# Kernel optimization log

Measured on AMD Instinct MI355X. Metric: run time of the kernel, lower is better.

## Reference

```python
import jax, jax.numpy as jnp
import numpy as np

B, T, F, H, P, HEADS = 1024, 128, 9, 256, 2048, 4
DH = H // HEADS

def _lstm_layer(x, Wih, Whh, bih, bhh):
    # x: [B,T,in]; gate order i,f,g,o (torch convention)
    xp = jnp.einsum('bti,gi->btg', x, Wih) + bih + bhh  # [B,T,4H]
    h0 = jnp.zeros((x.shape[0], Whh.shape[1]), x.dtype)
    def step(carry, xt):
        h, c = carry
        g = xt + h @ Whh.T
        i, f, gg, o = jnp.split(g, 4, axis=-1)
        c = jax.nn.sigmoid(f) * c + jax.nn.sigmoid(i) * jnp.tanh(gg)
        h = jax.nn.sigmoid(o) * jnp.tanh(c)
        return (h, c), h
    _, hs = jax.lax.scan(step, (h0, h0), jnp.swapaxes(xp, 0, 1))
    return jnp.swapaxes(hs, 0, 1)  # [B,T,H]

def _layernorm(x, g, b, eps=1e-5):
    mu = x.mean(-1, keepdims=True)
    var = ((x - mu) ** 2).mean(-1, keepdims=True)
    return (x - mu) * jax.lax.rsqrt(var + eps) * g + b

def setup_inputs():
    key = jax.random.key(0)
    ks = jax.random.split(key, 30)
    w = lambda k, s: jax.random.normal(k, s, jnp.float32) * 0.05
    return {
        'x': jax.random.normal(ks[0], (B, T, F), jnp.float32),
        'sku_indices': jnp.arange(B, dtype=jnp.int32),
        'adj': jax.random.uniform(ks[1], (P, P), jnp.float32),
        'vsn_emb_w': w(ks[2], (F, H)), 'vsn_emb_b': w(ks[3], (F, H)),
        'vsn_sel_w': w(ks[4], (F, F)), 'vsn_sel_b': w(ks[5], (F,)),
        'lstm_Wih0': w(ks[6], (4 * H, H)), 'lstm_Whh0': w(ks[7], (4 * H, H)),
        'lstm_bih0': w(ks[8], (4 * H,)), 'lstm_bhh0': w(ks[9], (4 * H,)),
        'lstm_Wih1': w(ks[10], (4 * H, H)), 'lstm_Whh1': w(ks[11], (4 * H, H)),
        'lstm_bih1': w(ks[12], (4 * H,)), 'lstm_bhh1': w(ks[13], (4 * H,)),
        'attn_in_w': w(ks[14], (3 * H, H)), 'attn_in_b': w(ks[15], (3 * H,)),
        'attn_out_w': w(ks[16], (H, H)), 'attn_out_b': w(ks[17], (H,)),
        'gnn_w': w(ks[18], (H, H)), 'gnn_b': w(ks[19], (H,)),
        'ln_g': jnp.ones((H,), jnp.float32), 'ln_b': jnp.zeros((H,), jnp.float32),
        'gate_w': w(ks[20], (H, 2 * H)), 'gate_b': w(ks[21], (H,)),
        'out_w': w(ks[22], (1, H)), 'out_b': w(ks[23], (1,)),
    }

def reference(x, sku_indices, adj, vsn_emb_w, vsn_emb_b, vsn_sel_w, vsn_sel_b,
              lstm_Wih0, lstm_Whh0, lstm_bih0, lstm_bhh0,
              lstm_Wih1, lstm_Whh1, lstm_bih1, lstm_bhh1,
              attn_in_w, attn_in_b, attn_out_w, attn_out_b,
              gnn_w, gnn_b, ln_g, ln_b, gate_w, gate_b, out_w, out_b):
    # --- TFT hidden: variable selection -> 2-layer LSTM -> MHA, take last step ---
    emb = x[..., None] * vsn_emb_w + vsn_emb_b           # [B,T,F,H]
    wts = jax.nn.softmax(x @ vsn_sel_w.T + vsn_sel_b, -1)  # [B,T,F]
    h = jnp.einsum('btf,btfh->bth', wts, emb)            # [B,T,H]
    h = _lstm_layer(h, lstm_Wih0, lstm_Whh0, lstm_bih0, lstm_bhh0)
    h = _lstm_layer(h, lstm_Wih1, lstm_Whh1, lstm_bih1, lstm_bhh1)
    qkv = h @ attn_in_w.T + attn_in_b                    # [B,T,3H]
    q, k, v = [a.reshape(B, T, HEADS, DH) for a in jnp.split(qkv, 3, axis=-1)]
    scores = jnp.einsum('bqhd,bkhd->bhqk', q, k) / np.sqrt(DH).astype(np.float32)
    attn = jax.nn.softmax(scores, -1)
    o = jnp.einsum('bhqk,bkhd->bqhd', attn, v).reshape(B, T, H)
    o = o @ attn_out_w.T + attn_out_b
    hidden = o[:, -1, :]                                  # [B,H]
    # --- GNN enrichment (all sku_indices valid here) ---
    product_embeds = jnp.zeros((P, H), hidden.dtype).at[sku_indices].set(hidden)
    degree = jnp.clip(adj.sum(1, keepdims=True), 1e-6)
    aggregated = (adj / degree) @ product_embeds          # [P,H]
    transformed = jax.nn.gelu(aggregated @ gnn_w.T + gnn_b, approximate=False)
    transformed = _layernorm(transformed, ln_g, ln_b)
    enriched = transformed[sku_indices]                   # [B,H]
    gate = jax.nn.sigmoid(jnp.concatenate([hidden, enriched], -1) @ gate_w.T + gate_b)
    combined = gate * enriched + (1.0 - gate) * hidden
    out = combined @ out_w.T + out_b                      # [B,1]
    return out.squeeze(-1)
```

## Files before the change

kernel.cpp:

```cpp
#include <hip/hip_runtime.h>
#include <hip/hip_fp16.h>

typedef _Float16 f16;
typedef _Float16 f16x8 __attribute__((ext_vector_type(8)));
typedef _Float16 f16x4 __attribute__((ext_vector_type(4)));
typedef float f32x4 __attribute__((ext_vector_type(4)));

#define B_ 1024
#define T_ 128
#define F_ 9
#define H_ 256
#define P_ 2048

__device__ __forceinline__ float sigf(float x) { return 1.f / (1.f + __expf(-x)); }
__device__ __forceinline__ float tanh_(float x) {
  float a = fminf(fabsf(x), 12.f);
  float e = __expf(2.f * a);
  float r = 1.f - 2.f / (e + 1.f);
  return copysignf(r, x);
}

__device__ __forceinline__ float blk_sum(float v) {
  __shared__ float sh[8];
  int lane = threadIdx.x & 63, w = threadIdx.x >> 6;
  int nw = blockDim.x >> 6;
#pragma unroll
  for (int o = 32; o > 0; o >>= 1) v += __shfl_xor(v, o, 64);
  __syncthreads();
  if (lane == 0) sh[w] = v;
  __syncthreads();
  float t = 0.f;
  for (int i = 0; i < nw; i++) t += sh[i];
  return t;
}

__global__ __launch_bounds__(256) void gemm_f16(
    const f16* __restrict__ A, int lda,
    const f16* __restrict__ Bt, int ldb,
    const float* __restrict__ bias,
    f16* __restrict__ o16, int ldo16,
    float* __restrict__ o32, int ldo32,
    int M, int N, int K)
{
  __shared__ __align__(16) f16 As[128][40];
  __shared__ __align__(16) f16 Bs[128][40];
  const int tid = threadIdx.x;
  const int lane = tid & 63, wave = tid >> 6;
  const int wr = (wave >> 1) * 64, wc = (wave & 1) * 64;
  const int q = lane >> 4, l15 = lane & 15;
  const int bm = blockIdx.x * 128, bn = blockIdx.y * 128;

  f32x4 acc[4][4];
#pragma unroll
  for (int i = 0; i < 4; i++)
#pragma unroll
    for (int j = 0; j < 4; j++) acc[i][j] = (f32x4){0.f, 0.f, 0.f, 0.f};

  for (int k0 = 0; k0 < K; k0 += 32) {
#pragma unroll
    for (int c = 0; c < 2; ++c) {
      int ch = tid + c * 256;
      int row = ch >> 2, kh = (ch & 3) * 8;
      *(f16x8*)&As[row][kh] = *(const f16x8*)&A[(size_t)(bm + row) * lda + k0 + kh];
      *(f16x8*)&Bs[row][kh] = *(const f16x8*)&Bt[(size_t)(bn + row) * ldb + k0 + kh];
    }
    __syncthreads();
    f16x8 af[4], bf[4];
#pragma unroll
    for (int tm = 0; tm < 4; tm++) af[tm] = *(const f16x8*)&As[wr + tm * 16 + l15][q * 8];
#pragma unroll
    for (int tn = 0; tn < 4; tn++) bf[tn] = *(const f16x8*)&Bs[wc + tn * 16 + l15][q * 8];
#pragma unroll
    for (int tm = 0; tm < 4; tm++)
#pragma unroll
      for (int tn = 0; tn < 4; tn++)
        acc[tm][tn] = __builtin_amdgcn_mfma_f32_16x16x32_f16(af[tm], bf[tn], acc[tm][tn], 0, 0, 0);
    __syncthreads();
  }
#pragma unroll
  for (int tm = 0; tm < 4; tm++) {
#pragma unroll
    for (int tn = 0; tn < 4; tn++) {
      int colg = bn + wc + tn * 16 + l15;
      float bv = bias ? bias[colg] : 0.f;
#pragma unroll
      for (int r = 0; r < 4; r++) {
        int rowg = bm + wr + tm * 16 + q * 4 + r;
        float v = acc[tm][tn][r] + bv;
        if (o32) o32[(size_t)rowg * ldo32 + colg] = v;
        if (o16) o16[(size_t)rowg * ldo16 + colg] = (f16)v;
      }
    }
  }
}

__global__ __launch_bounds__(256, 1) void lstm_sync(
    f16* __restrict__ hio,
    const f16* __restrict__ wpk,
    const float* __restrict__ bias,
    int* __restrict__ cnt)
{
  __shared__ __align__(16) f16 apf[16][64][8];
  __shared__ __align__(16) f16 htile[16][64];
  const int tid = threadIdx.x;
  const int lane = tid & 63, w = tid >> 6;
  const int q = lane >> 4, l15 = lane & 15;
  const int grp = blockIdx.x & 63, s = blockIdx.x >> 6;
  const int m0 = grp * 16;
  int* mycnt = cnt + grp * 64;

  f16x8 bf[4][16];
  {
    const f16* wbase = wpk + (((size_t)(s * 4 + w) * 4) * 16) * 512 + lane * 8;
#pragma unroll
    for (int g = 0; g < 4; g++)
#pragma unroll
      for (int k = 0; k < 16; k++)
        bf[g][k] = *(const f16x8*)(wbase + (size_t)(g * 16 + k) * 512);
  }
  float bv[4];
#pragma unroll
  for (int g = 0; g < 4; g++) bv[g] = bias[g * 256 + s * 64 + w * 16 + l15];

  const int srow = lane & 15, scb = lane >> 4;
  const size_t rowbase = ((size_t)(m0 + srow) * T_) * 256 + scb * 8;

  const f16x8 zv = {(f16)0, (f16)0, (f16)0, (f16)0, (f16)0, (f16)0, (f16)0, (f16)0};
  f16x8 xr0 = *(const f16x8*)&hio[rowbase + (size_t)w * 32];
  f16x8 xr1 = *(const f16x8*)&hio[rowbase + (size_t)(w + 4) * 32];
  float cst[4] = {0.f, 0.f, 0.f, 0.f};

  __syncthreads();
  if (tid == 0)
    __hip_atomic_fetch_add(mycnt, 1, __ATOMIC_RELAXED, __HIP_MEMORY_SCOPE_AGENT);

  for (int t = 0; t < T_; ++t) {
    if (tid == 0) {
      int it = 0;
      while (__hip_atomic_load(mycnt, __ATOMIC_RELAXED, __HIP_MEMORY_SCOPE_AGENT) < 4 * t + 4) {
        __builtin_amdgcn_s_sleep(1);
        if (++it > (1 << 26)) break;
      }
    }
    __syncthreads();
    *(f16x8*)&apf[w][lane][0]     = xr0;
    *(f16x8*)&apf[w + 4][lane][0] = xr1;
    f16x8 h0 = zv, h1 = zv;
    if (t > 0) {
      unsigned long long* p0 =
          (unsigned long long*)&hio[rowbase + (size_t)(t - 1) * 256 + (size_t)w * 32];
      unsigned long long* p1 =
          (unsigned long long*)&hio[rowbase + (size_t)(t - 1) * 256 + (size_t)(w + 4) * 32];
      union { unsigned long long u[2]; f16x8 v; } ua, ub;
      ua.u[0] = __hip_atomic_load(p0,     __ATOMIC_RELAXED, __HIP_MEMORY_SCOPE_AGENT);
      ua.u[1] = __hip_atomic_load(p0 + 1, __ATOMIC_RELAXED, __HIP_MEMORY_SCOPE_AGENT);
      ub.u[0] = __hip_atomic_load(p1,     __ATOMIC_RELAXED, __HIP_MEMORY_SCOPE_AGENT);
      ub.u[1] = __hip_atomic_load(p1 + 1, __ATOMIC_RELAXED, __HIP_MEMORY_SCOPE_AGENT);
      h0 = ua.v; h1 = ub.v;
    }
    *(f16x8*)&apf[8 + w][lane][0]  = h0;
    *(f16x8*)&apf[12 + w][lane][0] = h1;
    __syncthreads();

    f32x4 acc[4];
#pragma unroll
    for (int g = 0; g < 4; g++) acc[g] = (f32x4){0.f, 0.f, 0.f, 0.f};
#pragma unroll
    for (int k = 0; k < 16; k++) {
      f16x8 a = *(const f16x8*)&apf[k][lane][0];
#pragma unroll
      for (int g = 0; g < 4; g++)
        acc[g] = __builtin_amdgcn_mfma_f32_16x16x32_f16(a, bf[g][k], acc[g], 0, 0, 0);
    }
    if (t + 1 < T_) {
      xr0 = *(const f16x8*)&hio[rowbase + (size_t)(t + 1) * 256 + (size_t)w * 32];
      xr1 = *(const f16x8*)&hio[rowbase + (size_t)(t + 1) * 256 + (size_t)(w + 4) * 32];
    }
    f16 hn[4];
#pragma unroll
    for (int r = 0; r < 4; r++) {
      float ip = acc[0][r] + bv[0];
      float fp = acc[1][r] + bv[1];
      float gp = acc[2][r] + bv[2];
      float op = acc[3][r] + bv[3];
      float cn = sigf(fp) * cst[r] + sigf(ip) * tanh_(gp);
      cst[r] = cn;
      hn[r] = (f16)(sigf(op) * tanh_(cn));
    }
    __syncthreads();
#pragma unroll
    for (int r = 0; r < 4; r++) htile[q * 4 + r][w * 16 + l15] = hn[r];
    __syncthreads();
    {
      int row = tid >> 4, c4 = (tid & 15) * 4;
      union { unsigned long long u; f16x4 v; } uh;
      uh.v = *(const f16x4*)&htile[row][c4];
      __hip_atomic_store(
          (unsigned long long*)&hio[((size_t)(m0 + row) * T_ + t) * 256 + s * 64 + c4],
          uh.u, __ATOMIC_RELAXED, __HIP_MEMORY_SCOPE_AGENT);
    }
    __syncthreads();
    if (tid == 0)
      __hip_atomic_fetch_add(mycnt, 1, __ATOMIC_RELAXED, __HIP_MEMORY_SCOPE_AGENT);
  }
}

__global__ __launch_bounds__(256) void vsn_w_kernel(
    const float* __restrict__ x, const float* __restrict__ selw,
    const float* __restrict__ selb, float* __restrict__ wb)
{
  int pos = blockIdx.x * 256 + threadIdx.x;
  const float* xr = x + (size_t)pos * F_;
  float xv[F_];
#pragma unroll
  for (int f = 0; f < F_; f++) xv[f] = xr[f];
  float wv[F_]; float mx = -1e30f;
#pragma unroll
  for (int f = 0; f < F_; f++) {
    float s = selb[f];
#pragma unroll
    for (int f2 = 0; f2 < F_; f2++) s += xv[f2] * selw[f * F_ + f2];
    wv[f] = s; mx = fmaxf(mx, s);
  }
  float se = 0.f;
#pragma unroll
  for (int f = 0; f < F_; f++) { wv[f] = __expf(wv[f] - mx); se += wv[f]; }
  float inv = 1.f / se;
  float* o = wb + (size_t)pos * 18;
#pragma unroll
  for (int f = 0; f < F_; f++) {
    float wt = wv[f] * inv;
    o[f] = wt; o[9 + f] = wt * xv[f];
  }
}

__global__ __launch_bounds__(256) void vsn_h_kernel(
    const float* __restrict__ wb, const float* __restrict__ embw,
    const float* __restrict__ embb, f16* __restrict__ hout)
{
  int j = threadIdx.x;
  float ew[F_], eb[F_];
#pragma unroll
  for (int f = 0; f < F_; f++) { ew[f] = embw[f * H_ + j]; eb[f] = embb[f * H_ + j]; }
  for (int i = 0; i < 128; i++) {
    size_t pos = blockIdx.x + (size_t)i * 1024;
    const float* w = wb + pos * 18;
    float h = 0.f;
#pragma unroll
    for (int f = 0; f < F_; f++) h += w[9 + f] * ew[f] + w[f] * eb[f];
    hout[pos * H_ + j] = (f16)h;
  }
}

__global__ __launch_bounds__(256) void qk_kernel(
    const float* __restrict__ qbuf, const float* __restrict__ attn_in_w,
    float* __restrict__ qk)
{
  __shared__ float qs[256];
  int b = blockIdx.x, j = threadIdx.x;
  qs[j] = qbuf[(size_t)b * 256 + j];
  __syncthreads();
#pragma unroll
  for (int h = 0; h < 4; h++) {
    float acc = 0.f;
    for (int d = 0; d < 64; d++)
      acc += qs[h * 64 + d] * attn_in_w[(size_t)(256 + h * 64 + d) * 256 + j];
    qk[((size_t)b * 4 + h) * 256 + j] = acc * 0.125f;
  }
}

__global__ __launch_bounds__(256) void attnpool_kernel(
    const f16* __restrict__ hseq, const float* __restrict__ qk,
    float* __restrict__ hbar)
{
  __shared__ __align__(16) f16 hs[T_][264];
  __shared__ float qks[4][256];
  __shared__ float ps[4][T_];
  int b = blockIdx.x, tid = threadIdx.x;
  for (int i = tid; i < T_ * 32; i += 256) {
    int row = i >> 5, cc = (i & 31) * 8;
    *(f16x8*)&hs[row][cc] = *(const f16x8*)&hseq[((size_t)b * T_ + row) * 256 + cc];
  }
  for (int i = tid; i < 1024; i += 256) qks[i >> 8][i & 255] = qk[(size_t)b * 1024 + i];
  __syncthreads();
  if (tid < T_) {
    float s[4] = {0.f, 0.f, 0.f, 0.f};
    for (int cc = 0; cc < 32; cc++) {
      f16x8 v = *(const f16x8*)&hs[tid][cc * 8];
#pragma unroll
      for (int h = 0; h < 4; h++) {
        float a = 0.f;
#pragma unroll
        for (int j = 0; j < 8; j++) a += qks[h][cc * 8 + j] * (float)v[j];
        s[h] += a;
      }
    }
#pragma unroll
    for (int h = 0; h < 4; h++) ps[h][tid] = s[h];
  }
  __syncthreads();
  {
    int w = tid >> 6, l = tid & 63;
    float a = ps[w][l], bb = ps[w][l + 64];
    float m = fmaxf(a, bb);
#pragma unroll
    for (int o = 32; o > 0; o >>= 1) m = fmaxf(m, __shfl_xor(m, o, 64));
    float e0 = __expf(a - m), e1 = __expf(bb - m);
    float se = e0 + e1;
#pragma unroll
    for (int o = 32; o > 0; o >>= 1) se += __shfl_xor(se, o, 64);
    float inv = 1.f / se;
    ps[w][l] = e0 * inv; ps[w][l + 64] = e1 * inv;
  }
  __syncthreads();
  int j = tid;
  float acc[4] = {0.f, 0.f, 0.f, 0.f};
  for (int t = 0; t < T_; t++) {
    float hv = (float)hs[t][j];
#pragma unroll
    for (int h = 0; h < 4; h++) acc[h] += ps[h][t] * hv;
  }
#pragma unroll
  for (int h = 0; h < 4; h++) hbar[((size_t)b * 4 + h) * 256 + j] = acc[h];
}

__global__ __launch_bounds__(256) void vproj_kernel(
    const float* __restrict__ hbar, const float* __restrict__ attn_in_w,
    const float* __restrict__ attn_in_b, f16* __restrict__ aob)
{
  __shared__ float hb[4][256];
  int b = blockIdx.x, tid = threadIdx.x;
  for (int i = tid; i < 1024; i += 256) hb[i >> 8][i & 255] = hbar[(size_t)b * 1024 + i];
  __syncthreads();
  int d = tid, h = d >> 6;
  const float4* wr = (const float4*)(attn_in_w + (size_t)(512 + d) * 256);
  float acc = 0.f;
  for (int cc = 0; cc < 64; cc++) {
    float4 w4 = wr[cc];
    acc += w4.x * hb[h][cc * 4] + w4.y * hb[h][cc * 4 + 1]
         + w4.z * hb[h][cc * 4 + 2] + w4.w * hb[h][cc * 4 + 3];
  }
  aob[(size_t)b * 256 + d] = (f16)(acc + attn_in_b[512 + d]);
}

__global__ __launch_bounds__(256) void deg_adjn_kernel(
    const float* __restrict__ adj, const int* __restrict__ sku,
    f16* __restrict__ adjn)
{
  int bp = blockIdx.x;
  int p = sku[bp];
  int tid = threadIdx.x;
  float s = 0.f;
  for (int j = tid; j < P_; j += 256) s += adj[(size_t)p * P_ + j];
  float tot = blk_sum(s);
  float inv = 1.f / fmaxf(tot, 1e-6f);
  for (int b = tid; b < B_; b += 256)
    adjn[(size_t)bp * B_ + b] = (f16)(adj[(size_t)p * P_ + sku[b]] * inv);
}

__global__ void transpose_kernel(const float* __restrict__ hid, f16* __restrict__ hT)
{
  int i = blockIdx.x * 256 + threadIdx.x;
  int b = i >> 8, j = i & 255;
  hT[(size_t)j * B_ + b] = (f16)hid[i];
}

__global__ __launch_bounds__(256) void gelu_ln_kernel(
    const float* __restrict__ pre, const float* __restrict__ lg,
    const float* __restrict__ lb, float* __restrict__ enr,
    f16* __restrict__ hidcat)
{
  int row = blockIdx.x, j = threadIdx.x;
  float xv = pre[row * 256 + j];
  float ge = 0.5f * xv * (1.f + erff(xv * 0.70710678118654752f));
  float mu = blk_sum(ge) * (1.f / 256.f);
  float d = ge - mu;
  float var = blk_sum(d * d) * (1.f / 256.f);
  float y = d * rsqrtf(var + 1e-5f) * lg[j] + lb[j];
  enr[row * 256 + j] = y;
  hidcat[row * 512 + 256 + j] = (f16)y;
}

__global__ __launch_bounds__(256) void final_kernel(
    const float* __restrict__ gpre, const float* __restrict__ enr,
    const float* __restrict__ hid, const float* __restrict__ outw,
    const float* __restrict__ outb, float* __restrict__ out)
{
  int b = blockIdx.x, j = threadIdx.x;
  float gt = sigf(gpre[b * 256 + j]);
  float comb = gt * enr[b * 256 + j] + (1.f - gt) * hid[b * 256 + j];
  float v = comb * outw[j];
  float s = blk_sum(v);
  if (j == 0) out[b] = s + outb[0];
}

__global__ void prep_kernel(
    const float* Wih0, const float* Whh0, const float* Wih1, const float* Whh1,
    const float* bih0, const float* bhh0, const float* bih1, const float* bhh1,
    const float* attn_in_w, const float* attn_out_w, const float* gnn_w,
    const float* gate_w,
    f16* wpk0, f16* wpk1, f16* attninf, f16* attnoutf, f16* gnnwf, f16* gatewf,
    float* bias0, float* bias1)
{
  int idx = blockIdx.x * 256 + threadIdx.x;
  if (idx < 524288) {
    int j = idx & 7, lane = (idx >> 3) & 63, k = (idx >> 9) & 15;
    int g = (idx >> 13) & 3, w = (idx >> 15) & 3, s = (idx >> 17) & 3;
    int row = g * 256 + s * 64 + w * 16 + (lane & 15);
    int col = k * 32 + (lane >> 4) * 8 + j;
    float v0 = col < 256 ? Wih0[(size_t)row * 256 + col] : Whh0[(size_t)row * 256 + col - 256];
    float v1 = col < 256 ? Wih1[(size_t)row * 256 + col] : Whh1[(size_t)row * 256 + col - 256];
    wpk0[idx] = (f16)v0;
    wpk1[idx] = (f16)v1;
    return;
  }
  int i = idx - 524288;
  if (i < 65536) { attninf[i] = (f16)attn_in_w[i]; return; }
  i -= 65536;
  if (i < 65536) { attnoutf[i] = (f16)attn_out_w[i]; return; }
  i -= 65536;
  if (i < 65536) { gnnwf[i] = (f16)gnn_w[i]; return; }
  i -= 65536;
  if (i < 131072) { gatewf[i] = (f16)gate_w[i]; return; }
  i -= 131072;
  if (i < 1024) { bias0[i] = bih0[i] + bhh0[i]; return; }
  i -= 1024;
  if (i < 1024) { bias1[i] = bih1[i] + bhh1[i]; return; }
}

extern "C" void kernel_launch(void* const* d_in, const int* in_sizes, int n_in,
                              void* d_out, int out_size, void* d_ws, size_t ws_size,
                              hipStream_t stream)
{
  const float* x         = (const float*)d_in[0];
  const int*   sku       = (const int*)  d_in[1];
  const float* adj       = (const float*)d_in[2];
  const float* vsn_emb_w = (const float*)d_in[3];
  const float* vsn_emb_b = (const float*)d_in[4];
  const float* vsn_sel_w = (const float*)d_in[5];
  const float* vsn_sel_b = (const float*)d_in[6];
  const float* Wih0 = (const float*)d_in[7];
  const float* Whh0 = (const float*)d_in[8];
  const float* bih0 = (const float*)d_in[9];
  const float* bhh0 = (const float*)d_in[10];
  const float* Wih1 = (const float*)d_in[11];
  const float* Whh1 = (const float*)d_in[12];
  const float* bih1 = (const float*)d_in[13];
  const float* bhh1 = (const float*)d_in[14];
  const float* attn_in_w  = (const float*)d_in[15];
  const float* attn_in_b  = (const float*)d_in[16];
  const float* attn_out_w = (const float*)d_in[17];
  const float* attn_out_b = (const float*)d_in[18];
  const float* gnn_w  = (const float*)d_in[19];
  const float* gnn_b  = (const float*)d_in[20];
  const float* ln_g   = (const float*)d_in[21];
  const float* ln_b   = (const float*)d_in[22];
  const float* gate_w = (const float*)d_in[23];
  const float* gate_b = (const float*)d_in[24];
  const float* out_w  = (const float*)d_in[25];
  const float* out_b  = (const float*)d_in[26];
  (void)in_sizes; (void)n_in; (void)out_size; (void)ws_size;

  char* wsb = (char*)d_ws;
  size_t off = 0;
  auto alloc = [&](size_t bytes) -> void* {
    void* p = wsb + off;
    off += (bytes + 255) & ~(size_t)255;
    return p;
  };
  f16* hA      = (f16*)alloc((size_t)B_ * T_ * H_ * 2);
  f16* wpk0    = (f16*)alloc((size_t)1024 * 512 * 2);
  f16* wpk1    = (f16*)alloc((size_t)1024 * 512 * 2);
  f16* attninf = (f16*)alloc((size_t)256 * 256 * 2);
  f16* attnoutf= (f16*)alloc((size_t)256 * 256 * 2);
  f16* gnnwf   = (f16*)alloc((size_t)256 * 256 * 2);
  f16* gatewf  = (f16*)alloc((size_t)256 * 512 * 2);
  float* bias0 = (float*)alloc(1024 * 4);
  float* bias1 = (float*)alloc(1024 * 4);
  int* cnt0    = (int*)alloc(64 * 64 * 4);
  int* cnt1    = (int*)alloc(64 * 64 * 4);
  size_t off_tail = off;
  float* qbuf  = (float*)alloc((size_t)B_ * 256 * 4);
  float* qk    = (float*)alloc((size_t)B_ * 4 * 256 * 4);
  float* hbar  = (float*)alloc((size_t)B_ * 4 * 256 * 4);
  f16* aob     = (f16*)alloc((size_t)B_ * 256 * 2);
  float* hidden32 = (float*)alloc((size_t)B_ * 256 * 4);
  f16* hidcat  = (f16*)alloc((size_t)B_ * 512 * 2);
  f16* hT      = (f16*)alloc((size_t)256 * B_ * 2);
  f16* adjn    = (f16*)alloc((size_t)B_ * B_ * 2);
  f16* aggf    = (f16*)alloc((size_t)B_ * 256 * 2);
  float* gnnpre= (float*)alloc((size_t)B_ * 256 * 4);
  float* enr32 = (float*)alloc((size_t)B_ * 256 * 4);
  float* gatepre=(float*)alloc((size_t)B_ * 256 * 4);
  float* wb    = (float*)(wsb + off_tail);

  hipMemsetAsync(cnt0, 0, 2 * 64 * 64 * 4, stream);

  prep_kernel<<<3336, 256, 0, stream>>>(
      Wih0, Whh0, Wih1, Whh1, bih0, bhh0, bih1, bhh1,
      attn_in_w, attn_out_w, gnn_w, gate_w,
      wpk0, wpk1, attninf, attnoutf, gnnwf, gatewf, bias0, bias1);

  vsn_w_kernel<<<512, 256, 0, stream>>>(x, vsn_sel_w, vsn_sel_b, wb);
  vsn_h_kernel<<<1024, 256, 0, stream>>>(wb, vsn_emb_w, vsn_emb_b, hA);
  lstm_sync<<<256, 256, 0, stream>>>(hA, wpk0, bias0, cnt0);
  lstm_sync<<<256, 256, 0, stream>>>(hA, wpk1, bias1, cnt1);

  dim3 gS(B_ / 128, 256 / 128);
  gemm_f16<<<gS, 256, 0, stream>>>(hA + (size_t)(T_ - 1) * 256, T_ * 256, attninf, 256,
                                   attn_in_b, nullptr, 0, qbuf, 256, B_, 256, 256);
  qk_kernel<<<B_, 256, 0, stream>>>(qbuf, attn_in_w, qk);
  attnpool_kernel<<<B_, 256, 0, stream>>>(hA, qk, hbar);
  vproj_kernel<<<B_, 256, 0, stream>>>(hbar, attn_in_w, attn_in_b, aob);
  gemm_f16<<<gS, 256, 0, stream>>>(aob, 256, attnoutf, 256, attn_out_b,
                                   hidcat, 512, hidden32, 256, B_, 256, 256);
  deg_adjn_kernel<<<B_, 256, 0, stream>>>(adj, sku, adjn);
  transpose_kernel<<<B_, 256, 0, stream>>>(hidden32, hT);
  gemm_f16<<<gS, 256, 0, stream>>>(adjn, 1024, hT, 1024, nullptr,
                                   aggf, 256, nullptr, 0, B_, 256, 1024);
  gemm_f16<<<gS, 256, 0, stream>>>(aggf, 256, gnnwf, 256, gnn_b,
                                   nullptr, 0, gnnpre, 256, B_, 256, 256);
  gelu_ln_kernel<<<B_, 256, 0, stream>>>(gnnpre, ln_g, ln_b, enr32, hidcat);
  gemm_f16<<<gS, 256, 0, stream>>>(hidcat, 512, gatewf, 512, gate_b,
                                   nullptr, 0, gatepre, 256, B_, 256, 512);
  final_kernel<<<B_, 256, 0, stream>>>(gatepre, enr32, hidden32, out_w, out_b, (float*)d_out);
}
```

Before: 1.111 ms.

## Replace counter barrier in LSTM with poison-value dataflow sync on ping-pong buffers

The LSTM recurrence kernel previously synchronized the four column-slice blocks of each row group with an atomic counter barrier per timestep, plus extra __syncthreads. Now each layer reads input from one buffer and writes hidden states to a separate buffer that is pre-filled with 0xFF (a NaN pattern). Consumers spin on the h values themselves until no 64-bit word equals the poison pattern. This removes the counter atomics and two block barriers per step, and lets each wave proceed as soon as its own data arrives. In exchange it adds two full-size memsets of the hidden buffer and a second 32 MB buffer, and it assumes a legitimate f16 output never forms an all-ones 64-bit word.

New measurement: 1.206 ms. +8.6%, slower.

```diff
diff --git a/kernel.cpp b/kernel.cpp
--- a/kernel.cpp
+++ b/kernel.cpp
@@ -95,10 +95,10 @@
 }
 
 __global__ __launch_bounds__(256, 1) void lstm_sync(
-    f16* __restrict__ hio,
+    const f16* __restrict__ xin,
+    f16* __restrict__ hout,
     const f16* __restrict__ wpk,
-    const float* __restrict__ bias,
-    int* __restrict__ cnt)
+    const float* __restrict__ bias)
 {
   __shared__ __align__(16) f16 apf[16][64][8];
   __shared__ __align__(16) f16 htile[16][64];
@@ -107,7 +107,6 @@
   const int q = lane >> 4, l15 = lane & 15;
   const int grp = blockIdx.x & 63, s = blockIdx.x >> 6;
   const int m0 = grp * 16;
-  int* mycnt = cnt + grp * 64;
 
   f16x8 bf[4][16];
   {
@@ -126,38 +125,35 @@
   const size_t rowbase = ((size_t)(m0 + srow) * T_) * 256 + scb * 8;
 
   const f16x8 zv = {(f16)0, (f16)0, (f16)0, (f16)0, (f16)0, (f16)0, (f16)0, (f16)0};
-  f16x8 xr0 = *(const f16x8*)&hio[rowbase + (size_t)w * 32];
-  f16x8 xr1 = *(const f16x8*)&hio[rowbase + (size_t)(w + 4) * 32];
+  const unsigned long long POI = 0xFFFFFFFFFFFFFFFFull;
+
+  f16x8 xr0 = *(const f16x8*)&xin[rowbase + (size_t)w * 32];
+  f16x8 xr1 = *(const f16x8*)&xin[rowbase + (size_t)(w + 4) * 32];
   float cst[4] = {0.f, 0.f, 0.f, 0.f};
 
-  __syncthreads();
-  if (tid == 0)
-    __hip_atomic_fetch_add(mycnt, 1, __ATOMIC_RELAXED, __HIP_MEMORY_SCOPE_AGENT);
-
   for (int t = 0; t < T_; ++t) {
-    if (tid == 0) {
-      int it = 0;
-      while (__hip_atomic_load(mycnt, __ATOMIC_RELAXED, __HIP_MEMORY_SCOPE_AGENT) < 4 * t + 4) {
-        __builtin_amdgcn_s_sleep(1);
-        if (++it > (1 << 26)) break;
-      }
-    }
-    __syncthreads();
-    *(f16x8*)&apf[w][lane][0]     = xr0;
-    *(f16x8*)&apf[w + 4][lane][0] = xr1;
     f16x8 h0 = zv, h1 = zv;
     if (t > 0) {
       unsigned long long* p0 =
-          (unsigned long long*)&hio[rowbase + (size_t)(t - 1) * 256 + (size_t)w * 32];
+          (unsigned long long*)&hout[rowbase + (size_t)(t - 1) * 256 + (size_t)w * 32];
       unsigned long long* p1 =
-          (unsigned long long*)&hio[rowbase + (size_t)(t - 1) * 256 + (size_t)(w + 4) * 32];
+          (unsigned long long*)&hout[rowbase + (size_t)(t - 1) * 256 + (size_t)(w + 4) * 32];
       union { unsigned long long u[2]; f16x8 v; } ua, ub;
-      ua.u[0] = __hip_atomic_load(p0,     __ATOMIC_RELAXED, __HIP_MEMORY_SCOPE_AGENT);
-      ua.u[1] = __hip_atomic_load(p0 + 1, __ATOMIC_RELAXED, __HIP_MEMORY_SCOPE_AGENT);
-      ub.u[0] = __hip_atomic_load(p1,     __ATOMIC_RELAXED, __HIP_MEMORY_SCOPE_AGENT);
-      ub.u[1] = __hip_atomic_load(p1 + 1, __ATOMIC_RELAXED, __HIP_MEMORY_SCOPE_AGENT);
+      int it = 0;
+      for (;;) {
+        ua.u[0] = __hip_atomic_load(p0,     __ATOMIC_RELAXED, __HIP_MEMORY_SCOPE_AGENT);
+        ua.u[1] = __hip_atomic_load(p0 + 1, __ATOMIC_RELAXED, __HIP_MEMORY_SCOPE_AGENT);
+        ub.u[0] = __hip_atomic_load(p1,     __ATOMIC_RELAXED, __HIP_MEMORY_SCOPE_AGENT);
+        ub.u[1] = __hip_atomic_load(p1 + 1, __ATOMIC_RELAXED, __HIP_MEMORY_SCOPE_AGENT);
+        if (!((ua.u[0] == POI) | (ua.u[1] == POI) | (ub.u[0] == POI) | (ub.u[1] == POI)))
+          break;
+        if (++it > (1 << 24)) break;
+        __builtin_amdgcn_s_sleep(1);
+      }
       h0 = ua.v; h1 = ub.v;
     }
+    *(f16x8*)&apf[w][lane][0]      = xr0;
+    *(f16x8*)&apf[w + 4][lane][0]  = xr1;
     *(f16x8*)&apf[8 + w][lane][0]  = h0;
     *(f16x8*)&apf[12 + w][lane][0] = h1;
     __syncthreads();
@@ -173,8 +169,8 @@
         acc[g] = __builtin_amdgcn_mfma_f32_16x16x32_f16(a, bf[g][k], acc[g], 0, 0, 0);
     }
     if (t + 1 < T_) {
-      xr0 = *(const f16x8*)&hio[rowbase + (size_t)(t + 1) * 256 + (size_t)w * 32];
-      xr1 = *(const f16x8*)&hio[rowbase + (size_t)(t + 1) * 256 + (size_t)(w + 4) * 32];
+      xr0 = *(const f16x8*)&xin[rowbase + (size_t)(t + 1) * 256 + (size_t)w * 32];
+      xr1 = *(const f16x8*)&xin[rowbase + (size_t)(t + 1) * 256 + (size_t)(w + 4) * 32];
     }
     f16 hn[4];
 #pragma unroll
@@ -196,12 +192,9 @@
       union { unsigned long long u; f16x4 v; } uh;
       uh.v = *(const f16x4*)&htile[row][c4];
       __hip_atomic_store(
-          (unsigned long long*)&hio[((size_t)(m0 + row) * T_ + t) * 256 + s * 64 + c4],
+          (unsigned long long*)&hout[((size_t)(m0 + row) * T_ + t) * 256 + s * 64 + c4],
           uh.u, __ATOMIC_RELAXED, __HIP_MEMORY_SCOPE_AGENT);
     }
-    __syncthreads();
-    if (tid == 0)
-      __hip_atomic_fetch_add(mycnt, 1, __ATOMIC_RELAXED, __HIP_MEMORY_SCOPE_AGENT);
   }
 }
 
@@ -461,6 +454,8 @@
   const float* out_b  = (const float*)d_in[26];
   (void)in_sizes; (void)n_in; (void)out_size; (void)ws_size;
 
+  const size_t HBYTES = (size_t)B_ * T_ * H_ * 2;
+
   char* wsb = (char*)d_ws;
   size_t off = 0;
   auto alloc = [&](size_t bytes) -> void* {
@@ -468,7 +463,9 @@
     off += (bytes + 255) & ~(size_t)255;
     return p;
   };
-  f16* hA      = (f16*)alloc((size_t)B_ * T_ * H_ * 2);
+  f16* hA      = (f16*)alloc(HBYTES);
+  size_t off_hB = off;
+  f16* hB      = (f16*)alloc(HBYTES);
   f16* wpk0    = (f16*)alloc((size_t)1024 * 512 * 2);
   f16* wpk1    = (f16*)alloc((size_t)1024 * 512 * 2);
   f16* attninf = (f16*)alloc((size_t)256 * 256 * 2);
@@ -477,9 +474,8 @@
   f16* gatewf  = (f16*)alloc((size_t)256 * 512 * 2);
   float* bias0 = (float*)alloc(1024 * 4);
   float* bias1 = (float*)alloc(1024 * 4);
-  int* cnt0    = (int*)alloc(64 * 64 * 4);
-  int* cnt1    = (int*)alloc(64 * 64 * 4);
-  size_t off_tail = off;
+  off = off_hB;
+  float* wb    = (float*)alloc((size_t)B_ * T_ * 18 * 4);
   float* qbuf  = (float*)alloc((size_t)B_ * 256 * 4);
   float* qk    = (float*)alloc((size_t)B_ * 4 * 256 * 4);
   float* hbar  = (float*)alloc((size_t)B_ * 4 * 256 * 4);
@@ -492,9 +488,6 @@
   float* gnnpre= (float*)alloc((size_t)B_ * 256 * 4);
   float* enr32 = (float*)alloc((size_t)B_ * 256 * 4);
   float* gatepre=(float*)alloc((size_t)B_ * 256 * 4);
-  float* wb    = (float*)(wsb + off_tail);
-
-  hipMemsetAsync(cnt0, 0, 2 * 64 * 64 * 4, stream);
 
   prep_kernel<<<3336, 256, 0, stream>>>(
       Wih0, Whh0, Wih1, Whh1, bih0, bhh0, bih1, bhh1,
@@ -503,8 +496,10 @@
 
   vsn_w_kernel<<<512, 256, 0, stream>>>(x, vsn_sel_w, vsn_sel_b, wb);
   vsn_h_kernel<<<1024, 256, 0, stream>>>(wb, vsn_emb_w, vsn_emb_b, hA);
-  lstm_sync<<<256, 256, 0, stream>>>(hA, wpk0, bias0, cnt0);
-  lstm_sync<<<256, 256, 0, stream>>>(hA, wpk1, bias1, cnt1);
+  hipMemsetAsync(hB, 0xFF, HBYTES, stream);
+  lstm_sync<<<256, 256, 0, stream>>>(hA, hB, wpk0, bias0);
+  hipMemsetAsync(hA, 0xFF, HBYTES, stream);
+  lstm_sync<<<256, 256, 0, stream>>>(hB, hA, wpk1, bias1);
 
   dim3 gS(B_ / 128, 256 / 128);
   gemm_f16<<<gS, 256, 0, stream>>>(hA + (size_t)(T_ - 1) * 256, T_ * 256, attninf, 256,
```
